# Kernel optimization log

Hardware: AMD Instinct MI355X
Metric: run time of the kernel (lower is better)

Reference implementation:

```python
import jax, jax.numpy as jnp
import numpy as np

CLASSES = 4
THETA = 0.5


def setup_inputs() -> dict:
    key = jax.random.key(0)
    k1, k2 = jax.random.split(key)
    f = jax.random.normal(k1, (2, 32, 48, 48), dtype=jnp.float32)
    p = jax.random.normal(k2, (2, 4, 48, 48), dtype=jnp.float32)
    return {"f": f, "p": p}


def reference(f, p):
    k_p = CLASSES / float(np.log(CLASSES))
    B, Cf, H, W = f.shape
    N = H * W
    # softmax over class dim, drop background channel -> [B, P, H, W], P = classes-1
    p = jax.nn.softmax(p, axis=1)[:, 1:, :, :]
    P = p.shape[1]
    f = f.reshape(B, Cf, N)   # [B, Cf, N]
    p = p.reshape(B, P, N)    # [B, P, N]

    # per-pixel channel statistics (torch .std is unbiased -> ddof=1)
    mu = f.mean(axis=1)           # [B, N]
    std = f.std(axis=1, ddof=1)   # [B, N]

    # symmetric Gaussian KL between every pixel pair (i = loop pixel, j = all)
    dmu2 = (mu[:, :, None] - mu[:, None, :]) ** 2          # [B, N, N]
    si2 = (std ** 2)[:, :, None]
    sj2 = (std ** 2)[:, None, :]
    log_ratio = jnp.log(std[:, None, :] / std[:, :, None]) + jnp.log(std[:, :, None] / std[:, None, :])
    KL = 0.5 * (log_ratio + (si2 + dmu2) / (2.0 * sj2) + (sj2 + dmu2) / (2.0 * si2) - 1.0)

    # cosine similarity between every pixel pair
    gram = jnp.einsum('bci,bcj->bij', f, f)                # [B, N, N]
    norm2 = (f ** 2).sum(axis=1)                           # [B, N]
    cos = gram / jnp.sqrt(norm2[:, :, None] * norm2[:, None, :])

    dist = (KL + 2.0 * (1.0 - cos)) / 3.0                  # [B, N, N]
    Wmat = jnp.exp(-dist ** 2 / THETA ** 2)                # affinity kernel

    # probability compatibility and entropy weights
    pi = p[:, :, :, None]  # loop pixel i
    pj = p[:, :, None, :]  # all pixels j
    A = jnp.abs(2.0 * pj * pi) / (pj ** 2 + pi ** 2)       # [B, P, N, N]
    E = 1.0 + k_p * p * jnp.log(p)                         # [B, P, N]
    G = A * E[:, :, :, None] * E[:, :, None, :]            # [B, P, N, N]

    # sum over loop pixel i, then mean over [B, P, N]
    total = jnp.einsum('bij,bkij->', Wmat, G)
    score = total / (B * P * N)
    return 1.0 - score / N
```

## Files before the change

kernel.cpp:

```cpp
#include <hip/hip_runtime.h>

#define NPIX 2304
#define BB   2
#define CF   32
#define NP   3
#define TILE 64
#define NT   (NPIX / TILE)
#define NTRI (NT * (NT + 1) / 2)
#define KP   2.885390081777927f

__device__ __forceinline__ float frcp(float x) { return __builtin_amdgcn_rcpf(x); }

__global__ __launch_bounds__(256) void pair_kernel(const float* __restrict__ f,
                                                   const float* __restrict__ p,
                                                   double* __restrict__ partial) {
    __shared__ float sFi[CF][TILE];
    __shared__ float sFj[CF][TILE];
    __shared__ float sPi[10][TILE];
    __shared__ float sPj[10][TILE];

    const int b = blockIdx.y;
    int rem = blockIdx.x, ti = 0;
    while (rem >= NT - ti) { rem -= NT - ti; ++ti; }
    const int tj = ti + rem;
    const int i0 = ti * TILE, j0 = tj * TILE;
    const int tid = threadIdx.x;

    {
        const float* fb = f + (size_t)b * CF * NPIX;
        int col = tid & 63, c0 = tid >> 6;
        for (int c = c0; c < CF; c += 4) {
            sFi[c][col] = fb[(size_t)c * NPIX + i0 + col];
            sFj[c][col] = fb[(size_t)c * NPIX + j0 + col];
        }
    }
    __syncthreads();

    if (tid < 128) {
        const int side = tid >> 6;
        const int col  = tid & 63;
        const float (*sF)[TILE] = side ? sFj : sFi;
        float (*sP)[TILE]       = side ? sPj : sPi;
        const int base = (side ? j0 : i0) + col;

        float s1 = 0.f, s2 = 0.f;
#pragma unroll
        for (int c = 0; c < CF; ++c) {
            float v = sF[c][col];
            s1 += v;
            s2 = fmaf(v, v, s2);
        }
        float mu  = s1 * (1.0f / CF);
        float var = (s2 - s1 * s1 * (1.0f / CF)) * (1.0f / (CF - 1));
        sP[0][col] = mu;
        sP[1][col] = var;
        sP[2][col] = 0.5f / var;
        sP[3][col] = rsqrtf(s2);

        const float* pp = p + (size_t)b * 4 * NPIX + base;
        float x0 = pp[0], x1 = pp[NPIX], x2 = pp[2 * NPIX], x3 = pp[3 * NPIX];
        float m  = fmaxf(fmaxf(x0, x1), fmaxf(x2, x3));
        float e0 = expf(x0 - m), e1 = expf(x1 - m), e2 = expf(x2 - m), e3 = expf(x3 - m);
        float inv = 1.0f / (e0 + e1 + e2 + e3);
        float q[3] = { e1 * inv, e2 * inv, e3 * inv };
#pragma unroll
        for (int k = 0; k < 3; ++k) {
            float qq = q[k];
            float E  = 1.0f + KP * qq * logf(qq);
            sP[4 + k][col] = qq * E;
            sP[7 + k][col] = qq * qq;
        }
    }
    __syncthreads();

    const int tx = tid & 15;
    const int ty = tid >> 4;

    float accv[4][4];
#pragma unroll
    for (int m = 0; m < 4; ++m)
#pragma unroll
        for (int n = 0; n < 4; ++n) accv[m][n] = 0.f;

#pragma unroll 8
    for (int c = 0; c < CF; ++c) {
        const float4 a4 = *(const float4*)&sFi[c][ty * 4];
        const float4 b4 = *(const float4*)&sFj[c][tx * 4];
        float ai[4] = { a4.x, a4.y, a4.z, a4.w };
        float bj[4] = { b4.x, b4.y, b4.z, b4.w };
#pragma unroll
        for (int m = 0; m < 4; ++m)
#pragma unroll
            for (int n = 0; n < 4; ++n)
                accv[m][n] = fmaf(ai[m], bj[n], accv[m][n]);
    }

    float pj[10][4];
#pragma unroll
    for (int r = 0; r < 10; ++r)
#pragma unroll
        for (int n = 0; n < 4; ++n) pj[r][n] = sPj[r][tx * 4 + n];

    float fsum = 0.f;
#pragma unroll
    for (int m = 0; m < 4; ++m) {
        const int ii = ty * 4 + m;
        const float mu_i = sPi[0][ii], si2_i = sPi[1][ii];
        const float h_i  = sPi[2][ii], rn_i  = sPi[3][ii];
        const float u_i0 = sPi[4][ii], u_i1 = sPi[5][ii], u_i2 = sPi[6][ii];
        const float s_i0 = sPi[7][ii], s_i1 = sPi[8][ii], s_i2 = sPi[9][ii];
#pragma unroll
        for (int n = 0; n < 4; ++n) {
            const float d    = mu_i - pj[0][n];
            const float dmu2 = d * d;
            const float KL   = 0.5f * ((si2_i + dmu2) * pj[2][n] + (pj[1][n] + dmu2) * h_i - 1.0f);
            const float cosv = accv[m][n] * rn_i * pj[3][n];
            const float dist = (KL + 2.0f - 2.0f * cosv) * (1.0f / 3.0f);
            const float wm   = __expf(-4.0f * dist * dist);
            const float g = 2.0f * ( u_i0 * pj[4][n] * frcp(s_i0 + pj[7][n])
                                   + u_i1 * pj[5][n] * frcp(s_i1 + pj[8][n])
                                   + u_i2 * pj[6][n] * frcp(s_i2 + pj[9][n]) );
            fsum = fmaf(wm, g, fsum);
        }
    }

    double sum = (double)fsum;
    for (int off = 32; off; off >>= 1) sum += __shfl_down(sum, off);
    __shared__ double wsumd[4];
    const int lane = tid & 63, wid = tid >> 6;
    if (lane == 0) wsumd[wid] = sum;
    __syncthreads();
    if (tid == 0) {
        const double wgt = (ti == tj) ? 1.0 : 2.0;
        partial[(size_t)b * NTRI + blockIdx.x] =
            ((wsumd[0] + wsumd[1]) + (wsumd[2] + wsumd[3])) * wgt;
    }
}

__global__ __launch_bounds__(256) void finalize_kernel(const double* __restrict__ partial,
                                                       float* __restrict__ out) {
    double s = 0.0;
    for (int i = threadIdx.x; i < BB * NTRI; i += 256) s += partial[i];
    for (int off = 32; off; off >>= 1) s += __shfl_down(s, off);
    __shared__ double wsumd[4];
    const int lane = threadIdx.x & 63, wid = threadIdx.x >> 6;
    if (lane == 0) wsumd[wid] = s;
    __syncthreads();
    if (threadIdx.x == 0) {
        double total = (wsumd[0] + wsumd[1]) + (wsumd[2] + wsumd[3]);
        out[0] = (float)(1.0 - total / ((double)BB * NP * (double)NPIX * (double)NPIX));
    }
}

extern "C" void kernel_launch(void* const* d_in, const int* in_sizes, int n_in,
                              void* d_out, int out_size, void* d_ws, size_t ws_size,
                              hipStream_t stream) {
    const float* f = (const float*)d_in[0];
    const float* p = (const float*)d_in[1];
    double* partial = (double*)d_ws;
    float*  out     = (float*)d_out;

    dim3 grid(NTRI, BB);
    pair_kernel<<<grid, 256, 0, stream>>>(f, p, partial);
    finalize_kernel<<<1, 256, 0, stream>>>(partial, out);
}
```

Baseline: 71.06 us.

## Fold finalize into pair kernel via last-block atomic; prenormalize features

Replaces the separate finalize kernel with a last-block-done pattern: each block writes its partial, fences, bumps an atomic counter, and the final block reduces all partials and writes the output. A memset of the counter is added before the launch. Separately, features are scaled by the inverse norm in shared memory so the Gram accumulation directly yields cosine, which removes one shared-memory row and two multiplies per pair. This trades one kernel launch for a memset plus an atomic per block.

```diff
diff --git a/kernel.cpp b/kernel.cpp
--- a/kernel.cpp
+++ b/kernel.cpp
@@ -7,17 +7,20 @@
 #define TILE 64
 #define NT   (NPIX / TILE)
 #define NTRI (NT * (NT + 1) / 2)
+#define NBLK (NTRI * BB)
 #define KP   2.885390081777927f
 
 __device__ __forceinline__ float frcp(float x) { return __builtin_amdgcn_rcpf(x); }
 
 __global__ __launch_bounds__(256) void pair_kernel(const float* __restrict__ f,
                                                    const float* __restrict__ p,
-                                                   double* __restrict__ partial) {
+                                                   double* __restrict__ partial,
+                                                   unsigned int* __restrict__ counter,
+                                                   float* __restrict__ out) {
     __shared__ float sFi[CF][TILE];
     __shared__ float sFj[CF][TILE];
-    __shared__ float sPi[10][TILE];
-    __shared__ float sPj[10][TILE];
+    __shared__ float sPi[9][TILE];
+    __shared__ float sPj[9][TILE];
 
     const int b = blockIdx.y;
     int rem = blockIdx.x, ti = 0;
@@ -39,8 +42,8 @@
     if (tid < 128) {
         const int side = tid >> 6;
         const int col  = tid & 63;
-        const float (*sF)[TILE] = side ? sFj : sFi;
-        float (*sP)[TILE]       = side ? sPj : sPi;
+        float (*sF)[TILE] = side ? sFj : sFi;
+        float (*sP)[TILE] = side ? sPj : sPi;
         const int base = (side ? j0 : i0) + col;
 
         float s1 = 0.f, s2 = 0.f;
@@ -52,10 +55,12 @@
         }
         float mu  = s1 * (1.0f / CF);
         float var = (s2 - s1 * s1 * (1.0f / CF)) * (1.0f / (CF - 1));
+        float rn  = rsqrtf(s2);
         sP[0][col] = mu;
         sP[1][col] = var;
         sP[2][col] = 0.5f / var;
-        sP[3][col] = rsqrtf(s2);
+#pragma unroll
+        for (int c = 0; c < CF; ++c) sF[c][col] *= rn;
 
         const float* pp = p + (size_t)b * 4 * NPIX + base;
         float x0 = pp[0], x1 = pp[NPIX], x2 = pp[2 * NPIX], x3 = pp[3 * NPIX];
@@ -67,8 +72,8 @@
         for (int k = 0; k < 3; ++k) {
             float qq = q[k];
             float E  = 1.0f + KP * qq * logf(qq);
-            sP[4 + k][col] = qq * E;
-            sP[7 + k][col] = qq * qq;
+            sP[3 + k][col] = qq * E;
+            sP[6 + k][col] = qq * qq;
         }
     }
     __syncthreads();
@@ -95,9 +100,9 @@
                 accv[m][n] = fmaf(ai[m], bj[n], accv[m][n]);
     }
 
-    float pj[10][4];
+    float pj[9][4];
 #pragma unroll
-    for (int r = 0; r < 10; ++r)
+    for (int r = 0; r < 9; ++r)
 #pragma unroll
         for (int n = 0; n < 4; ++n) pj[r][n] = sPj[r][tx * 4 + n];
 
@@ -105,21 +110,19 @@
 #pragma unroll
     for (int m = 0; m < 4; ++m) {
         const int ii = ty * 4 + m;
-        const float mu_i = sPi[0][ii], si2_i = sPi[1][ii];
-        const float h_i  = sPi[2][ii], rn_i  = sPi[3][ii];
-        const float u_i0 = sPi[4][ii], u_i1 = sPi[5][ii], u_i2 = sPi[6][ii];
-        const float s_i0 = sPi[7][ii], s_i1 = sPi[8][ii], s_i2 = sPi[9][ii];
+        const float mu_i = sPi[0][ii], si2_i = sPi[1][ii], h_i = sPi[2][ii];
+        const float u_i0 = sPi[3][ii], u_i1 = sPi[4][ii], u_i2 = sPi[5][ii];
+        const float s_i0 = sPi[6][ii], s_i1 = sPi[7][ii], s_i2 = sPi[8][ii];
 #pragma unroll
         for (int n = 0; n < 4; ++n) {
             const float d    = mu_i - pj[0][n];
             const float dmu2 = d * d;
             const float KL   = 0.5f * ((si2_i + dmu2) * pj[2][n] + (pj[1][n] + dmu2) * h_i - 1.0f);
-            const float cosv = accv[m][n] * rn_i * pj[3][n];
-            const float dist = (KL + 2.0f - 2.0f * cosv) * (1.0f / 3.0f);
+            const float dist = (KL + 2.0f - 2.0f * accv[m][n]) * (1.0f / 3.0f);
             const float wm   = __expf(-4.0f * dist * dist);
-            const float g = 2.0f * ( u_i0 * pj[4][n] * frcp(s_i0 + pj[7][n])
-                                   + u_i1 * pj[5][n] * frcp(s_i1 + pj[8][n])
-                                   + u_i2 * pj[6][n] * frcp(s_i2 + pj[9][n]) );
+            const float g = 2.0f * ( u_i0 * pj[3][n] * frcp(s_i0 + pj[6][n])
+                                   + u_i1 * pj[4][n] * frcp(s_i1 + pj[7][n])
+                                   + u_i2 * pj[5][n] * frcp(s_i2 + pj[8][n]) );
             fsum = fmaf(wm, g, fsum);
         }
     }
@@ -130,25 +133,30 @@
     const int lane = tid & 63, wid = tid >> 6;
     if (lane == 0) wsumd[wid] = sum;
     __syncthreads();
+
+    __shared__ unsigned int isLast;
     if (tid == 0) {
         const double wgt = (ti == tj) ? 1.0 : 2.0;
         partial[(size_t)b * NTRI + blockIdx.x] =
             ((wsumd[0] + wsumd[1]) + (wsumd[2] + wsumd[3])) * wgt;
+        __threadfence();
+        unsigned int old = atomicAdd(counter, 1u);
+        isLast = (old == (unsigned int)(NBLK - 1)) ? 1u : 0u;
     }
-}
+    __syncthreads();
 
-__global__ __launch_bounds__(256) void finalize_kernel(const double* __restrict__ partial,
-                                                       float* __restrict__ out) {
-    double s = 0.0;
-    for (int i = threadIdx.x; i < BB * NTRI; i += 256) s += partial[i];
-    for (int off = 32; off; off >>= 1) s += __shfl_down(s, off);
-    __shared__ double wsumd[4];
-    const int lane = threadIdx.x & 63, wid = threadIdx.x >> 6;
-    if (lane == 0) wsumd[wid] = s;
-    __syncthreads();
-    if (threadIdx.x == 0) {
-        double total = (wsumd[0] + wsumd[1]) + (wsumd[2] + wsumd[3]);
-        out[0] = (float)(1.0 - total / ((double)BB * NP * (double)NPIX * (double)NPIX));
+    if (isLast) {
+        __threadfence();
+        double s = 0.0;
+        for (int i = tid; i < NBLK; i += 256) s += partial[i];
+        for (int off = 32; off; off >>= 1) s += __shfl_down(s, off);
+        __shared__ double fsumd[4];
+        if (lane == 0) fsumd[wid] = s;
+        __syncthreads();
+        if (tid == 0) {
+            double total = (fsumd[0] + fsumd[1]) + (fsumd[2] + fsumd[3]);
+            out[0] = (float)(1.0 - total / ((double)BB * NP * (double)NPIX * (double)NPIX));
+        }
     }
 }
 
@@ -157,10 +165,11 @@
                               hipStream_t stream) {
     const float* f = (const float*)d_in[0];
     const float* p = (const float*)d_in[1];
-    double* partial = (double*)d_ws;
-    float*  out     = (float*)d_out;
+    double*       partial = (double*)d_ws;
+    unsigned int* counter = (unsigned int*)((char*)d_ws + 10752);
+    float*        out     = (float*)d_out;
 
+    hipMemsetAsync(counter, 0, sizeof(unsigned int), stream);
     dim3 grid(NTRI, BB);
-    pair_kernel<<<grid, 256, 0, stream>>>(f, p, partial);
-    finalize_kernel<<<1, 256, 0, stream>>>(partial, out);
+    pair_kernel<<<grid, 256, 0, stream>>>(f, p, partial, counter, out);
 }
```

After: 90.64 us. +27.5%, slower.
